# Optimization experiments

Hardware: AMD Instinct MI355X
Metric: run time of the kernel (lower is better)

## Reference

```python
import jax, jax.numpy as jnp
import numpy as np


def segment_softmax(logits, seg, num_seg):
    m = jax.ops.segment_max(logits, seg, num_segments=num_seg)
    z = jnp.exp(logits - m[seg])
    s = jax.ops.segment_sum(z, seg, num_segments=num_seg)
    return z / s[seg]


def hconv(x_lin, edge_node, edge_he, num_nodes, num_edges, bias, alpha=None):
    # PyG HypergraphConv (heads=1, concat=True): D^-1 H W_e B^-1 H^T X Theta
    ones = jnp.ones(edge_node.shape[0], x_lin.dtype)
    D = jax.ops.segment_sum(ones, edge_node, num_segments=num_nodes)
    Dinv = jnp.where(D > 0, 1.0 / D, 0.0)
    Bd = jax.ops.segment_sum(ones, edge_he, num_segments=num_edges)
    Binv = jnp.where(Bd > 0, 1.0 / Bd, 0.0)
    # node -> hyperedge
    msg = Binv[edge_he][:, None] * x_lin[edge_node]
    if alpha is not None:
        msg = alpha[:, None] * msg
    e = jax.ops.segment_sum(msg, edge_he, num_segments=num_edges)
    # hyperedge -> node
    msg2 = Dinv[edge_node][:, None] * e[edge_he]
    if alpha is not None:
        msg2 = alpha[:, None] * msg2
    out = jax.ops.segment_sum(msg2, edge_node, num_segments=num_nodes)
    return out + bias


def reference(c_it, medicine_it, c_embeddings, m_embeddings, W_conv, b_conv, W_gat, att, b_gat, he_attr):
    nd = c_embeddings.shape[0]  # all indicators are 1 -> nonzero indexing is identity
    nm = m_embeddings.shape[0]
    oc = W_conv.shape[0]

    # diagnosis hypergraph: single hyperedge containing all diseases
    dia_x = c_embeddings @ W_conv.T  # [nd, oc]
    dia_nf = hconv(dia_x, jnp.arange(nd), jnp.zeros(nd, jnp.int32), nd, 1, b_conv)

    # medicine hypergraph: single hyperedge containing all medicines
    med_x = m_embeddings @ W_conv.T  # [nm, oc]
    med_nf = hconv(med_x, jnp.arange(nm), jnp.zeros(nm, jnp.int32), nm, 1, b_conv)

    # dia-med hypergraph: nd hyperedges, hyperedge d = {disease d} U {all medicines}
    comb = jnp.concatenate([c_embeddings, m_embeddings], axis=0)  # [nd+nm, in]
    x_lin = comb @ W_gat.T                                        # [nd+nm, oc]
    he_lin = he_attr @ W_gat.T                                    # [nd, oc]
    med_nodes = jnp.arange(nd, nd + nm)
    edge_node = jnp.concatenate(
        [jnp.arange(nd)[:, None], jnp.broadcast_to(med_nodes[None, :], (nd, nm))], axis=1
    ).reshape(-1)                              # [nd*(nm+1)]
    edge_he = jnp.repeat(jnp.arange(nd), nm + 1)

    # attention (attention_mode='node'): alpha from source node + hyperedge attr, softmax per hyperedge
    a_node = x_lin @ att[:oc]   # [nd+nm]
    a_he = he_lin @ att[oc:]    # [nd]
    logits = jax.nn.leaky_relu(a_node[edge_node] + a_he[edge_he], 0.2)
    alpha = segment_softmax(logits, edge_he, nd)

    dm_nf = hconv(x_lin, edge_node, edge_he, nd + nm, nd, b_gat, alpha)  # [nd+nm, oc]

    disease_final = jnp.concatenate([dm_nf[:nd], dia_nf], axis=1)   # [nd, 2*oc]
    medicine_final = jnp.concatenate([dm_nf[nd:], med_nf], axis=1)  # [nm, 2*oc]
    return jnp.concatenate([disease_final, medicine_final], axis=0)  # [nd+nm, 2*oc]


def setup_inputs() -> dict:
    key = jax.random.key(0)
    ks = jax.random.split(key, 8)
    ND, NM, IN, OUT = 2048, 512, 256, 128
    s = 0.05
    return {
        "c_it": jnp.ones((ND,), jnp.int32),
        "medicine_it": jnp.ones((NM,), jnp.int32),
        "c_embeddings": jax.random.normal(ks[0], (ND, IN), jnp.float32),
        "m_embeddings": jax.random.normal(ks[1], (NM, IN), jnp.float32),
        "W_conv": jax.random.normal(ks[2], (OUT, IN), jnp.float32) * s,
        "b_conv": jax.random.normal(ks[3], (OUT,), jnp.float32) * s,
        "W_gat": jax.random.normal(ks[4], (OUT, IN), jnp.float32) * s,
        "att": jax.random.normal(ks[5], (2 * OUT,), jnp.float32) * s,
        "b_gat": jax.random.normal(ks[6], (OUT,), jnp.float32) * s,
        "he_attr": jax.random.normal(ks[7], (ND, IN), jnp.float32),
    }
```

## Files before the change

kernel.cpp:

```cpp
#include <hip/hip_runtime.h>

#define ND 2048
#define NM 512
#define DIN 256
#define OC 128
#define NTOT 2560
#define NE 513

#define WS_PARTC 0
#define WS_PARTM (WS_PARTC + 256*256)
#define WS_AHE   (WS_PARTM + 64*256)
#define WS_ANODE (WS_AHE + ND)
#define WS_CD    (WS_ANODE + NTOT)
#define WS_XLIN  (WS_CD + ND)
#define WS_DIA   (WS_XLIN + NTOT*OC)
#define WS_MED   (WS_DIA + OC)
#define WS_E16   (WS_MED + OC)

typedef unsigned short u16;
typedef unsigned int u32;

__device__ __forceinline__ float lrelu(float x) { return x > 0.f ? x : 0.2f * x; }
__device__ __forceinline__ u16 f2b(float f) {
    u32 x = __float_as_uint(f);
    return (u16)((x + 0x7fffu + ((x >> 16) & 1u)) >> 16);
}
__device__ __forceinline__ float bfl(u32 u) { return __uint_as_float(u << 16); }
__device__ __forceinline__ float bfh(u32 u) { return __uint_as_float(u & 0xffff0000u); }

__global__ void __launch_bounds__(256) K1(
        const float* __restrict__ c_emb, const float* __restrict__ m_emb,
        const float* __restrict__ W_gat, const float* __restrict__ att,
        const float* __restrict__ he_attr, float* __restrict__ ws) {
    const int b = blockIdx.x, t = threadIdx.x;
    if (b < 320) {
        __shared__ float row[8][DIN];
        __shared__ float sA[8][OC];
        const int d0 = b * 8;
#pragma unroll
        for (int p = 0; p < 4; ++p) {
            const int idx = p * 256 + t;
            const int r = idx >> 7, c = idx & 127;
            const int d = d0 + r;
            const float* src = (d < ND) ? c_emb + (size_t)d * DIN
                                        : m_emb + (size_t)(d - ND) * DIN;
            const float2 u = ((const float2*)src)[c];
            row[r][2 * c]     = u.x;
            row[r][2 * c + 1] = u.y;
        }
        __syncthreads();
        {
            float pc = 0.f;
#pragma unroll
            for (int r = 0; r < 8; ++r) pc += row[r][t];
            if (b < 256) ws[WS_PARTC + b * 256 + t] = pc;
            else         ws[WS_PARTM + (b - 256) * 256 + t] = pc;
        }
        const int o = t & (OC - 1), h = t >> 7;
        float a0 = 0.f, a1 = 0.f, a2 = 0.f, a3 = 0.f;
        const float4* wr  = (const float4*)(W_gat + (size_t)o * DIN);
        const float4* r0v = (const float4*)(row[4 * h]);
        const float4* r1v = (const float4*)(row[4 * h + 1]);
        const float4* r2v = (const float4*)(row[4 * h + 2]);
        const float4* r3v = (const float4*)(row[4 * h + 3]);
#pragma unroll 4
        for (int v = 0; v < 64; ++v) {
            const float4 w  = wr[v];
            const float4 x0 = r0v[v], x1 = r1v[v], x2 = r2v[v], x3 = r3v[v];
            a0 = fmaf(x0.x, w.x, a0); a0 = fmaf(x0.y, w.y, a0);
            a0 = fmaf(x0.z, w.z, a0); a0 = fmaf(x0.w, w.w, a0);
            a1 = fmaf(x1.x, w.x, a1); a1 = fmaf(x1.y, w.y, a1);
            a1 = fmaf(x1.z, w.z, a1); a1 = fmaf(x1.w, w.w, a1);
            a2 = fmaf(x2.x, w.x, a2); a2 = fmaf(x2.y, w.y, a2);
            a2 = fmaf(x2.z, w.z, a2); a2 = fmaf(x2.w, w.w, a2);
            a3 = fmaf(x3.x, w.x, a3); a3 = fmaf(x3.y, w.y, a3);
            a3 = fmaf(x3.z, w.z, a3); a3 = fmaf(x3.w, w.w, a3);
        }
        float* xl = ws + WS_XLIN + (size_t)(d0 + 4 * h) * OC + o;
        xl[0 * OC] = a0; xl[1 * OC] = a1; xl[2 * OC] = a2; xl[3 * OC] = a3;
        const float at = att[o];
        sA[4 * h][o]     = a0 * at;
        sA[4 * h + 1][o] = a1 * at;
        sA[4 * h + 2][o] = a2 * at;
        sA[4 * h + 3][o] = a3 * at;
        __syncthreads();
#pragma unroll
        for (int st = 64; st >= 1; st >>= 1) {
            for (int idx = t; idx < 8 * st; idx += 256) {
                const int r = idx / st, i = idx - r * st;
                sA[r][i] += sA[r][i + st];
            }
            __syncthreads();
        }
        if (t < 8) ws[WS_ANODE + d0 + t] = sA[t][0];
    } else {
        __shared__ float satt[OC];
        __shared__ float we[DIN];
        const int q = b - 320;
        if (t < OC) satt[t] = att[OC + t];
        __syncthreads();
        float acc = 0.f;
#pragma unroll 8
        for (int o = 0; o < OC; ++o)
            acc = fmaf(W_gat[(size_t)o * DIN + t], satt[o], acc);
        we[t] = acc;
        __syncthreads();
        const int r = t >> 5, l = t & 31;
#pragma unroll
        for (int k = 0; k < 4; ++k) {
            const int d = q * 32 + k * 8 + r;
            const float* he = he_attr + (size_t)d * DIN;
            float ah = 0.f;
#pragma unroll
            for (int i = l; i < DIN; i += 32) ah = fmaf(he[i], we[i], ah);
#pragma unroll
            for (int m = 1; m < 32; m <<= 1) ah += __shfl_xor(ah, m, 32);
            if (l == 0) ws[WS_AHE + d] = ah;
        }
    }
}

__global__ void __launch_bounds__(256) K2(
        const float* __restrict__ W_conv, const float* __restrict__ b_conv,
        const float* __restrict__ b_gat, float* __restrict__ ws,
        float* __restrict__ out) {
    const int b = blockIdx.x, t = threadIdx.x;
    if (b == 256) {
        __shared__ float mc[DIN], mm[DIN];
        float sc = 0.f, sm = 0.f;
        for (int bb = 0; bb < 256; ++bb) sc += ws[WS_PARTC + bb * 256 + t];
        for (int bb = 0; bb < 64;  ++bb) sm += ws[WS_PARTM + bb * 256 + t];
        mc[t] = sc * (1.f / ND);
        mm[t] = sm * (1.f / NM);
        __syncthreads();
        if (t < OC) {
            const float4* wr = (const float4*)(W_conv + (size_t)t * DIN);
            float a = 0.f, m2 = 0.f;
#pragma unroll 8
            for (int v = 0; v < 64; ++v) {
                const float4 w = wr[v];
                const int ib = 4 * v;
                a  = fmaf(mc[ib], w.x, a);      a  = fmaf(mc[ib + 1], w.y, a);
                a  = fmaf(mc[ib + 2], w.z, a);  a  = fmaf(mc[ib + 3], w.w, a);
                m2 = fmaf(mm[ib], w.x, m2);     m2 = fmaf(mm[ib + 1], w.y, m2);
                m2 = fmaf(mm[ib + 2], w.z, m2); m2 = fmaf(mm[ib + 3], w.w, m2);
            }
            const float bc = b_conv[t];
            ws[WS_DIA + t] = a + bc;
            ws[WS_MED + t] = m2 + bc;
        }
        return;
    }
    __shared__ float zbuf[NE][8];
    __shared__ float anm[NM];
    __shared__ float sacc[8][8][OC];
    anm[t]       = ws[WS_ANODE + ND + t];
    anm[t + 256] = ws[WS_ANODE + ND + 256 + t];
    __syncthreads();
    {
        const int r = t >> 5, l = t & 31;
        const int d = b * 8 + r;
        const float ah = ws[WS_AHE + d];
        const float an_d = ws[WS_ANODE + d];
        float lmax = -3.4e38f;
        for (int j = l; j < NE; j += 32) {
            const float v = (j == 0) ? an_d : anm[j - 1];
            const float lg = lrelu(v + ah);
            zbuf[j][r] = lg;
            lmax = fmaxf(lmax, lg);
        }
#pragma unroll
        for (int m = 1; m < 32; m <<= 1) lmax = fmaxf(lmax, __shfl_xor(lmax, m, 32));
        float ss = 0.f;
        for (int j = l; j < NE; j += 32) {
            const float z = __expf(zbuf[j][r] - lmax);
            zbuf[j][r] = z;
            ss += z;
        }
#pragma unroll
        for (int m = 1; m < 32; m <<= 1) ss += __shfl_xor(ss, m, 32);
        const float inv = 1.f / ss;
        if (l == 0) ws[WS_CD + d] = lmax + __logf(ss);
        for (int j = l; j < NE; j += 32) zbuf[j][r] *= inv;
    }
    __syncthreads();
    {
        const int q = t & 31, s = t >> 5;
        const float4* xm4 = (const float4*)(ws + WS_XLIN + (size_t)ND * OC);
        float4 acc[8];
#pragma unroll
        for (int k = 0; k < 8; ++k) acc[k] = make_float4(0.f, 0.f, 0.f, 0.f);
        const int j0 = s * 64;
#pragma unroll 4
        for (int i = 0; i < 64; ++i) {
            const int j = j0 + i;
            const float4 ev = xm4[(size_t)j * 32 + q];
            const float4* zr = (const float4*)zbuf[j + 1];
            const float4 za = zr[0], zb4 = zr[1];
            acc[0].x = fmaf(za.x, ev.x, acc[0].x); acc[0].y = fmaf(za.x, ev.y, acc[0].y);
            acc[0].z = fmaf(za.x, ev.z, acc[0].z); acc[0].w = fmaf(za.x, ev.w, acc[0].w);
            acc[1].x = fmaf(za.y, ev.x, acc[1].x); acc[1].y = fmaf(za.y, ev.y, acc[1].y);
            acc[1].z = fmaf(za.y, ev.z, acc[1].z); acc[1].w = fmaf(za.y, ev.w, acc[1].w);
            acc[2].x = fmaf(za.z, ev.x, acc[2].x); acc[2].y = fmaf(za.z, ev.y, acc[2].y);
            acc[2].z = fmaf(za.z, ev.z, acc[2].z); acc[2].w = fmaf(za.z, ev.w, acc[2].w);
            acc[3].x = fmaf(za.w, ev.x, acc[3].x); acc[3].y = fmaf(za.w, ev.y, acc[3].y);
            acc[3].z = fmaf(za.w, ev.z, acc[3].z); acc[3].w = fmaf(za.w, ev.w, acc[3].w);
            acc[4].x = fmaf(zb4.x, ev.x, acc[4].x); acc[4].y = fmaf(zb4.x, ev.y, acc[4].y);
            acc[4].z = fmaf(zb4.x, ev.z, acc[4].z); acc[4].w = fmaf(zb4.x, ev.w, acc[4].w);
            acc[5].x = fmaf(zb4.y, ev.x, acc[5].x); acc[5].y = fmaf(zb4.y, ev.y, acc[5].y);
            acc[5].z = fmaf(zb4.y, ev.z, acc[5].z); acc[5].w = fmaf(zb4.y, ev.w, acc[5].w);
            acc[6].x = fmaf(zb4.z, ev.x, acc[6].x); acc[6].y = fmaf(zb4.z, ev.y, acc[6].y);
            acc[6].z = fmaf(zb4.z, ev.z, acc[6].z); acc[6].w = fmaf(zb4.z, ev.w, acc[6].w);
            acc[7].x = fmaf(zb4.w, ev.x, acc[7].x); acc[7].y = fmaf(zb4.w, ev.y, acc[7].y);
            acc[7].z = fmaf(zb4.w, ev.z, acc[7].z); acc[7].w = fmaf(zb4.w, ev.w, acc[7].w);
        }
#pragma unroll
        for (int k = 0; k < 8; ++k) ((float4*)sacc[s][k])[q] = acc[k];
    }
    __syncthreads();
    {
        u16* e16 = (u16*)(ws + WS_E16);
        for (int idx = t; idx < 8 * OC; idx += 256) {
            const int k = idx >> 7, o = idx & 127;
            const int dd = b * 8 + k;
            float sum = 0.f;
#pragma unroll
            for (int s2 = 0; s2 < 8; ++s2) sum += sacc[s2][k][o];
            const float a0 = zbuf[0][k];
            const float xown = ws[WS_XLIN + (size_t)dd * OC + o];
            const float ev = fmaf(a0, xown, sum) * (1.f / NE);
            e16[(size_t)dd * OC + o] = f2b(ev);
            out[(size_t)dd * 2 * OC + o] = fmaf(a0, ev, b_gat[o]);
        }
    }
}

__global__ void __launch_bounds__(256) K3(
        const float* __restrict__ b_gat, const float* __restrict__ ws,
        float* __restrict__ out) {
    const int b = blockIdx.x, t = threadIdx.x;
    if (b < 256) {
        __shared__ float zb[ND][2];
        __shared__ float sacc[16][2][OC];
        const int m0 = b * 2;
        const float an0 = ws[WS_ANODE + ND + m0];
        const float an1 = ws[WS_ANODE + ND + m0 + 1];
        for (int dd = t; dd < ND; dd += 256) {
            const float ahv = ws[WS_AHE + dd];
            const float cdv = ws[WS_CD + dd];
            zb[dd][0] = __expf(lrelu(an0 + ahv) - cdv);
            zb[dd][1] = __expf(lrelu(an1 + ahv) - cdv);
        }
        __syncthreads();
        const int q = t & 15, s = t >> 4;
        const uint4* e4 = (const uint4*)((const u16*)(ws + WS_E16));
        float A0[8] = {0, 0, 0, 0, 0, 0, 0, 0};
        float A1[8] = {0, 0, 0, 0, 0, 0, 0, 0};
        const int dd0 = s * 128;
#pragma unroll 4
        for (int i = 0; i < 128; ++i) {
            const int dd = dd0 + i;
            const uint4 u = e4[(size_t)dd * 16 + q];
            const float z0 = zb[dd][0], z1 = zb[dd][1];
            const float e0 = bfl(u.x), e1 = bfh(u.x);
            const float e2 = bfl(u.y), e3 = bfh(u.y);
            const float e4v = bfl(u.z), e5 = bfh(u.z);
            const float e6 = bfl(u.w), e7 = bfh(u.w);
            A0[0] = fmaf(z0, e0, A0[0]); A0[1] = fmaf(z0, e1, A0[1]);
            A0[2] = fmaf(z0, e2, A0[2]); A0[3] = fmaf(z0, e3, A0[3]);
            A0[4] = fmaf(z0, e4v, A0[4]); A0[5] = fmaf(z0, e5, A0[5]);
            A0[6] = fmaf(z0, e6, A0[6]); A0[7] = fmaf(z0, e7, A0[7]);
            A1[0] = fmaf(z1, e0, A1[0]); A1[1] = fmaf(z1, e1, A1[1]);
            A1[2] = fmaf(z1, e2, A1[2]); A1[3] = fmaf(z1, e3, A1[3]);
            A1[4] = fmaf(z1, e4v, A1[4]); A1[5] = fmaf(z1, e5, A1[5]);
            A1[6] = fmaf(z1, e6, A1[6]); A1[7] = fmaf(z1, e7, A1[7]);
        }
#pragma unroll
        for (int i = 0; i < 8; ++i) {
            sacc[s][0][q * 8 + i] = A0[i];
            sacc[s][1][q * 8 + i] = A1[i];
        }
        __syncthreads();
        const int med = t >> 7, o = t & 127;
        float sum = 0.f;
#pragma unroll
        for (int sl = 0; sl < 16; ++sl) sum += sacc[sl][med][o];
        const int m = m0 + med;
        out[(size_t)(ND + m) * 2 * OC + o]      = fmaf(sum, 1.f / ND, b_gat[o]);
        out[(size_t)(ND + m) * 2 * OC + OC + o] = ws[WS_MED + o];
    } else {
        const int q2 = b - 256;
        const int o = t & (OC - 1), h = t >> 7;
        const float dv = ws[WS_DIA + o];
#pragma unroll
        for (int rr = 0; rr < 16; ++rr) {
            const int d = q2 * 32 + 2 * rr + h;
            out[(size_t)d * 2 * OC + OC + o] = dv;
        }
    }
}

extern "C" void kernel_launch(void* const* d_in, const int* in_sizes, int n_in,
                              void* d_out, int out_size, void* d_ws, size_t ws_size,
                              hipStream_t stream) {
    const float* c_emb   = (const float*)d_in[2];
    const float* m_emb   = (const float*)d_in[3];
    const float* W_conv  = (const float*)d_in[4];
    const float* b_conv  = (const float*)d_in[5];
    const float* W_gat   = (const float*)d_in[6];
    const float* att     = (const float*)d_in[7];
    const float* b_gat   = (const float*)d_in[8];
    const float* he_attr = (const float*)d_in[9];
    float* ws  = (float*)d_ws;
    float* out = (float*)d_out;

    hipLaunchKernelGGL(K1, dim3(384), dim3(256), 0, stream,
                       c_emb, m_emb, W_gat, att, he_attr, ws);
    hipLaunchKernelGGL(K2, dim3(257), dim3(256), 0, stream,
                       W_conv, b_conv, b_gat, ws, out);
    hipLaunchKernelGGL(K3, dim3(320), dim3(256), 0, stream, b_gat, ws, out);
}
```

Before: 124.0 us.

## Store medicine projections in bf16 and process four medicines per K3 block

Medicine rows of x_lin are now written as bf16 into a separate workspace buffer, and K2's aggregation reads them as packed uint4 with 16 slices instead of float4 with 8 slices. This halves the bytes read for the medicine features, at the cost of precision in the hyperedge sums. K3 now handles four medicines per block instead of two, halving how many times the shared bf16 hyperedge matrix is read, with fewer blocks launched and more registers per thread.

After: 135.2 us. +9.1%, slower.

```diff
diff --git a/kernel.cpp b/kernel.cpp
--- a/kernel.cpp
+++ b/kernel.cpp
@@ -13,9 +13,10 @@
 #define WS_ANODE (WS_AHE + ND)
 #define WS_CD    (WS_ANODE + NTOT)
 #define WS_XLIN  (WS_CD + ND)
-#define WS_DIA   (WS_XLIN + NTOT*OC)
+#define WS_DIA   (WS_XLIN + ND*OC)
 #define WS_MED   (WS_DIA + OC)
-#define WS_E16   (WS_MED + OC)
+#define WS_XM16  (WS_MED + OC)
+#define WS_E16   (WS_XM16 + NM*OC/2)
 
 typedef unsigned short u16;
 typedef unsigned int u32;
@@ -76,8 +77,17 @@
             a3 = fmaf(x3.x, w.x, a3); a3 = fmaf(x3.y, w.y, a3);
             a3 = fmaf(x3.z, w.z, a3); a3 = fmaf(x3.w, w.w, a3);
         }
-        float* xl = ws + WS_XLIN + (size_t)(d0 + 4 * h) * OC + o;
-        xl[0 * OC] = a0; xl[1 * OC] = a1; xl[2 * OC] = a2; xl[3 * OC] = a3;
+        if (b < 256) {
+            float* xl = ws + WS_XLIN + (size_t)(d0 + 4 * h) * OC + o;
+            xl[0 * OC] = a0; xl[1 * OC] = a1; xl[2 * OC] = a2; xl[3 * OC] = a3;
+        } else {
+            const int m0 = d0 - ND + 4 * h;
+            u16* xm16 = (u16*)(ws + WS_XM16);
+            xm16[(size_t)(m0 + 0) * OC + o] = f2b(a0);
+            xm16[(size_t)(m0 + 1) * OC + o] = f2b(a1);
+            xm16[(size_t)(m0 + 2) * OC + o] = f2b(a2);
+            xm16[(size_t)(m0 + 3) * OC + o] = f2b(a3);
+        }
         const float at = att[o];
         sA[4 * h][o]     = a0 * at;
         sA[4 * h + 1][o] = a1 * at;
@@ -153,7 +163,7 @@
     }
     __shared__ float zbuf[NE][8];
     __shared__ float anm[NM];
-    __shared__ float sacc[8][8][OC];
+    __shared__ float sacc[16][8][OC];
     anm[t]       = ws[WS_ANODE + ND + t];
     anm[t + 256] = ws[WS_ANODE + ND + 256 + t];
     __syncthreads();
@@ -185,37 +195,36 @@
     }
     __syncthreads();
     {
-        const int q = t & 31, s = t >> 5;
-        const float4* xm4 = (const float4*)(ws + WS_XLIN + (size_t)ND * OC);
-        float4 acc[8];
-#pragma unroll
-        for (int k = 0; k < 8; ++k) acc[k] = make_float4(0.f, 0.f, 0.f, 0.f);
-        const int j0 = s * 64;
+        const int q = t & 15, s = t >> 4;
+        const uint4* xm4 = (const uint4*)((const u16*)(ws + WS_XM16));
+        float acc[8][8];
+#pragma unroll
+        for (int k = 0; k < 8; ++k)
+#pragma unroll
+            for (int i = 0; i < 8; ++i) acc[k][i] = 0.f;
+        const int j0 = s * 32;
 #pragma unroll 4
-        for (int i = 0; i < 64; ++i) {
+        for (int i = 0; i < 32; ++i) {
             const int j = j0 + i;
-            const float4 ev = xm4[(size_t)j * 32 + q];
+            const uint4 u = xm4[(size_t)j * 16 + q];
+            float ev[8];
+            ev[0] = bfl(u.x); ev[1] = bfh(u.x);
+            ev[2] = bfl(u.y); ev[3] = bfh(u.y);
+            ev[4] = bfl(u.z); ev[5] = bfh(u.z);
+            ev[6] = bfl(u.w); ev[7] = bfh(u.w);
             const float4* zr = (const float4*)zbuf[j + 1];
             const float4 za = zr[0], zb4 = zr[1];
-            acc[0].x = fmaf(za.x, ev.x, acc[0].x); acc[0].y = fmaf(za.x, ev.y, acc[0].y);
-            acc[0].z = fmaf(za.x, ev.z, acc[0].z); acc[0].w = fmaf(za.x, ev.w, acc[0].w);
-            acc[1].x = fmaf(za.y, ev.x, acc[1].x); acc[1].y = fmaf(za.y, ev.y, acc[1].y);
-            acc[1].z = fmaf(za.y, ev.z, acc[1].z); acc[1].w = fmaf(za.y, ev.w, acc[1].w);
-            acc[2].x = fmaf(za.z, ev.x, acc[2].x); acc[2].y = fmaf(za.z, ev.y, acc[2].y);
-            acc[2].z = fmaf(za.z, ev.z, acc[2].z); acc[2].w = fmaf(za.z, ev.w, acc[2].w);
-            acc[3].x = fmaf(za.w, ev.x, acc[3].x); acc[3].y = fmaf(za.w, ev.y, acc[3].y);
-            acc[3].z = fmaf(za.w, ev.z, acc[3].z); acc[3].w = fmaf(za.w, ev.w, acc[3].w);
-            acc[4].x = fmaf(zb4.x, ev.x, acc[4].x); acc[4].y = fmaf(zb4.x, ev.y, acc[4].y);
-            acc[4].z = fmaf(zb4.x, ev.z, acc[4].z); acc[4].w = fmaf(zb4.x, ev.w, acc[4].w);
-            acc[5].x = fmaf(zb4.y, ev.x, acc[5].x); acc[5].y = fmaf(zb4.y, ev.y, acc[5].y);
-            acc[5].z = fmaf(zb4.y, ev.z, acc[5].z); acc[5].w = fmaf(zb4.y, ev.w, acc[5].w);
-            acc[6].x = fmaf(zb4.z, ev.x, acc[6].x); acc[6].y = fmaf(zb4.z, ev.y, acc[6].y);
-            acc[6].z = fmaf(zb4.z, ev.z, acc[6].z); acc[6].w = fmaf(zb4.z, ev.w, acc[6].w);
-            acc[7].x = fmaf(zb4.w, ev.x, acc[7].x); acc[7].y = fmaf(zb4.w, ev.y, acc[7].y);
-            acc[7].z = fmaf(zb4.w, ev.z, acc[7].z); acc[7].w = fmaf(zb4.w, ev.w, acc[7].w);
-        }
-#pragma unroll
-        for (int k = 0; k < 8; ++k) ((float4*)sacc[s][k])[q] = acc[k];
+            const float zk[8] = {za.x, za.y, za.z, za.w, zb4.x, zb4.y, zb4.z, zb4.w};
+#pragma unroll
+            for (int k = 0; k < 8; ++k)
+#pragma unroll
+                for (int oi = 0; oi < 8; ++oi)
+                    acc[k][oi] = fmaf(zk[k], ev[oi], acc[k][oi]);
+        }
+#pragma unroll
+        for (int k = 0; k < 8; ++k)
+#pragma unroll
+            for (int oi = 0; oi < 8; ++oi) sacc[s][k][q * 8 + oi] = acc[k][oi];
     }
     __syncthreads();
     {
@@ -225,7 +234,7 @@
             const int dd = b * 8 + k;
             float sum = 0.f;
 #pragma unroll
-            for (int s2 = 0; s2 < 8; ++s2) sum += sacc[s2][k][o];
+            for (int s2 = 0; s2 < 16; ++s2) sum += sacc[s2][k][o];
             const float a0 = zbuf[0][k];
             const float xown = ws[WS_XLIN + (size_t)dd * OC + o];
             const float ev = fmaf(a0, xown, sum) * (1.f / NE);
@@ -239,57 +248,62 @@
         const float* __restrict__ b_gat, const float* __restrict__ ws,
         float* __restrict__ out) {
     const int b = blockIdx.x, t = threadIdx.x;
-    if (b < 256) {
-        __shared__ float zb[ND][2];
-        __shared__ float sacc[16][2][OC];
-        const int m0 = b * 2;
-        const float an0 = ws[WS_ANODE + ND + m0];
-        const float an1 = ws[WS_ANODE + ND + m0 + 1];
+    if (b < 128) {
+        __shared__ float zb[ND][4];
+        __shared__ float sacc[16][4][OC];
+        const int m0 = b * 4;
+        float an[4];
+#pragma unroll
+        for (int k = 0; k < 4; ++k) an[k] = ws[WS_ANODE + ND + m0 + k];
         for (int dd = t; dd < ND; dd += 256) {
             const float ahv = ws[WS_AHE + dd];
             const float cdv = ws[WS_CD + dd];
-            zb[dd][0] = __expf(lrelu(an0 + ahv) - cdv);
-            zb[dd][1] = __expf(lrelu(an1 + ahv) - cdv);
+#pragma unroll
+            for (int k = 0; k < 4; ++k)
+                zb[dd][k] = __expf(lrelu(an[k] + ahv) - cdv);
         }
         __syncthreads();
         const int q = t & 15, s = t >> 4;
         const uint4* e4 = (const uint4*)((const u16*)(ws + WS_E16));
-        float A0[8] = {0, 0, 0, 0, 0, 0, 0, 0};
-        float A1[8] = {0, 0, 0, 0, 0, 0, 0, 0};
+        float A[4][8];
+#pragma unroll
+        for (int k = 0; k < 4; ++k)
+#pragma unroll
+            for (int i = 0; i < 8; ++i) A[k][i] = 0.f;
         const int dd0 = s * 128;
 #pragma unroll 4
         for (int i = 0; i < 128; ++i) {
             const int dd = dd0 + i;
             const uint4 u = e4[(size_t)dd * 16 + q];
-            const float z0 = zb[dd][0], z1 = zb[dd][1];
-            const float e0 = bfl(u.x), e1 = bfh(u.x);
-            const float e2 = bfl(u.y), e3 = bfh(u.y);
-            const float e4v = bfl(u.z), e5 = bfh(u.z);
-            const float e6 = bfl(u.w), e7 = bfh(u.w);
-            A0[0] = fmaf(z0, e0, A0[0]); A0[1] = fmaf(z0, e1, A0[1]);
-            A0[2] = fmaf(z0, e2, A0[2]); A0[3] = fmaf(z0, e3, A0[3]);
-            A0[4] = fmaf(z0, e4v, A0[4]); A0[5] = fmaf(z0, e5, A0[5]);
-            A0[6] = fmaf(z0, e6, A0[6]); A0[7] = fmaf(z0, e7, A0[7]);
-            A1[0] = fmaf(z1, e0, A1[0]); A1[1] = fmaf(z1, e1, A1[1]);
-            A1[2] = fmaf(z1, e2, A1[2]); A1[3] = fmaf(z1, e3, A1[3]);
-            A1[4] = fmaf(z1, e4v, A1[4]); A1[5] = fmaf(z1, e5, A1[5]);
-            A1[6] = fmaf(z1, e6, A1[6]); A1[7] = fmaf(z1, e7, A1[7]);
-        }
-#pragma unroll
-        for (int i = 0; i < 8; ++i) {
-            sacc[s][0][q * 8 + i] = A0[i];
-            sacc[s][1][q * 8 + i] = A1[i];
-        }
-        __syncthreads();
-        const int med = t >> 7, o = t & 127;
-        float sum = 0.f;
-#pragma unroll
-        for (int sl = 0; sl < 16; ++sl) sum += sacc[sl][med][o];
-        const int m = m0 + med;
-        out[(size_t)(ND + m) * 2 * OC + o]      = fmaf(sum, 1.f / ND, b_gat[o]);
-        out[(size_t)(ND + m) * 2 * OC + OC + o] = ws[WS_MED + o];
+            float ev[8];
+            ev[0] = bfl(u.x); ev[1] = bfh(u.x);
+            ev[2] = bfl(u.y); ev[3] = bfh(u.y);
+            ev[4] = bfl(u.z); ev[5] = bfh(u.z);
+            ev[6] = bfl(u.w); ev[7] = bfh(u.w);
+            const float4 zq = *(const float4*)zb[dd];
+            const float zk[4] = {zq.x, zq.y, zq.z, zq.w};
+#pragma unroll
+            for (int k = 0; k < 4; ++k)
+#pragma unroll
+                for (int oi = 0; oi < 8; ++oi)
+                    A[k][oi] = fmaf(zk[k], ev[oi], A[k][oi]);
+        }
+#pragma unroll
+        for (int k = 0; k < 4; ++k)
+#pragma unroll
+            for (int oi = 0; oi < 8; ++oi) sacc[s][k][q * 8 + oi] = A[k][oi];
+        __syncthreads();
+        for (int idx = t; idx < 4 * OC; idx += 256) {
+            const int med = idx >> 7, o = idx & 127;
+            float sum = 0.f;
+#pragma unroll
+            for (int sl = 0; sl < 16; ++sl) sum += sacc[sl][med][o];
+            const int m = m0 + med;
+            out[(size_t)(ND + m) * 2 * OC + o]      = fmaf(sum, 1.f / ND, b_gat[o]);
+            out[(size_t)(ND + m) * 2 * OC + OC + o] = ws[WS_MED + o];
+        }
     } else {
-        const int q2 = b - 256;
+        const int q2 = b - 128;
         const int o = t & (OC - 1), h = t >> 7;
         const float dv = ws[WS_DIA + o];
 #pragma unroll
@@ -318,5 +332,5 @@
                        c_emb, m_emb, W_gat, att, he_attr, ws);
     hipLaunchKernelGGL(K2, dim3(257), dim3(256), 0, stream,
                        W_conv, b_conv, b_gat, ws, out);
-    hipLaunchKernelGGL(K3, dim3(320), dim3(256), 0, stream, b_gat, ws, out);
-}
+    hipLaunchKernelGGL(K3, dim3(192), dim3(256), 0, stream, b_gat, ws, out);
+}
```
